# Optimization experiments

Hardware: AMD Instinct MI355X
Metric: run time of the kernel (lower is better)

The kernel has to match this reference:

```python
import jax, jax.numpy as jnp
import numpy as np

H = 16
D_MODEL = 1024
D_K = D_MODEL // H


def setup_inputs() -> dict:
    key = jax.random.key(0)
    ks = jax.random.split(key, 8)
    B, S = 4, 2048
    query = jax.random.normal(ks[0], (B, S, D_MODEL), dtype=jnp.float32)
    key_t = jax.random.normal(ks[1], (B, S, D_MODEL), dtype=jnp.float32)
    value = jax.random.normal(ks[2], (B, S, D_MODEL), dtype=jnp.float32)
    mask = jax.random.randint(ks[3], (B, S, S), 0, 2, dtype=jnp.int32)
    sc = 1.0 / np.sqrt(D_MODEL)
    Wq = jax.random.normal(ks[4], (D_MODEL, D_MODEL), dtype=jnp.float32) * sc
    Wk = jax.random.normal(ks[5], (D_MODEL, D_MODEL), dtype=jnp.float32) * sc
    Wv = jax.random.normal(ks[6], (D_MODEL, D_MODEL), dtype=jnp.float32) * sc
    Wo = jax.random.normal(ks[7], (D_MODEL, D_MODEL), dtype=jnp.float32) * sc
    return {"query": query, "key": key_t, "value": value, "mask": mask,
            "Wq": Wq, "Wk": Wk, "Wv": Wv, "Wo": Wo}


def reference(query, key, value, mask, Wq, Wk, Wv, Wo):
    B, S, _ = query.shape
    # nn.Linear(bias=False): y = x @ W^T; then split heads -> [B,H,S,d_k]
    def proj(x, W):
        return (x @ W.T).reshape(B, S, H, D_K).transpose(0, 2, 1, 3)

    q = proj(query, Wq)
    k = proj(key, Wk)
    v = proj(value, Wv)

    m = (mask[:, None, :, :] != 0)  # [B,1,S,S] broadcast over heads
    scores = jnp.einsum('bhqd,bhkd->bhqk', q, k) / jnp.sqrt(jnp.float32(D_K))
    scores = jnp.where(m, scores, jnp.float32(-1e9))
    p_attn = jax.nn.softmax(scores, axis=-1)
    p_attn = jnp.where(m, p_attn, 0.0)
    # dropout is identity in eval mode
    x = jnp.einsum('bhqk,bhkd->bhqd', p_attn, v)
    x = x.transpose(0, 2, 1, 3).reshape(B, S, D_MODEL)
    return x @ Wo.T
```

## Files before the change

kernel.cpp:

```cpp
#include <hip/hip_runtime.h>


typedef __attribute__((ext_vector_type(8))) short frag8;
typedef __attribute__((ext_vector_type(4))) float f32x4;
typedef unsigned long long ull;

#define MFMA16(a,b,c) __builtin_amdgcn_mfma_f32_16x16x32_bf16((a),(b),(c),0,0,0)

__device__ __forceinline__ short f2bf(float f) {
  union { float f; unsigned u; } x; x.f = f;
  unsigned r = (x.u + 0x7fffu + ((x.u >> 16) & 1u)) >> 16;
  return (short)r;
}

__device__ __forceinline__ unsigned pkbf(float lo, float hi) {
  union { float f; unsigned u; } a, b;
  a.f = lo; b.f = hi;
  return __builtin_amdgcn_perm(b.u + 0x8000u, a.u + 0x8000u, 0x07060302u);
}

__device__ __forceinline__ void gl16(const void* g, void* l) {
  __builtin_amdgcn_global_load_lds(
      (const __attribute__((address_space(1))) unsigned*)g,
      (__attribute__((address_space(3))) unsigned*)l, 16, 0, 0);
}

__global__ __launch_bounds__(256) void cast_qkv(
    const float* __restrict__ q, const float* __restrict__ k,
    const float* __restrict__ v, short* __restrict__ qo,
    short* __restrict__ ko, short* __restrict__ vo) {
  int z = blockIdx.x >> 13;
  int i = (blockIdx.x & 8191) * 256 + threadIdx.x;
  const float* s = z == 0 ? q : z == 1 ? k : v;
  short* d = z == 0 ? qo : z == 1 ? ko : vo;
  float4 f = ((const float4*)s)[i];
  short4 o;
  o.x = f2bf(f.x); o.y = f2bf(f.y); o.z = f2bf(f.z); o.w = f2bf(f.w);
  ((short4*)d)[i] = o;
}

__global__ __launch_bounds__(256) void cast_w(
    const float* __restrict__ wq, const float* __restrict__ wk,
    const float* __restrict__ wv, const float* __restrict__ wo,
    short* __restrict__ oq, short* __restrict__ ok,
    short* __restrict__ ov, short* __restrict__ oo) {
  int z = blockIdx.x >> 10;
  int i = (blockIdx.x & 1023) * 256 + threadIdx.x;
  const float* s = z == 0 ? wq : z == 1 ? wk : z == 2 ? wv : wo;
  short* d = z == 0 ? oq : z == 1 ? ok : z == 2 ? ov : oo;
  float sc = (z == 0) ? 0.18033688011f : 1.0f;
  float4 f = ((const float4*)s)[i];
  short4 o;
  o.x = f2bf(f.x * sc); o.y = f2bf(f.y * sc);
  o.z = f2bf(f.z * sc); o.w = f2bf(f.w * sc);
  ((short4*)d)[i] = o;
}

__global__ __launch_bounds__(256) void pack_mask(
    const int* __restrict__ mask, ull* __restrict__ bits) {
  int wv = threadIdx.x >> 6, l = threadIdx.x & 63;
  size_t row = (size_t)blockIdx.x * 4 + wv;
  const int* src = mask + row * 2048;
  for (int c = 0; c < 2048; c += 64) {
    ull bl = __ballot(src[c + l] != 0);
    if (l == 0) bits[row * 32 + (c >> 6)] = bl;
  }
}

template <int MODE>
__device__ __forceinline__ void gemm_body(const short* __restrict__ A,
                                          const short* __restrict__ W,
                                          void* __restrict__ outp, int bid) {
  __shared__ short As[2][128 * 32];
  __shared__ short Bs[2][128 * 32];
  const int t = threadIdx.x;
  const int l = t & 63, wv = t >> 6;
  const int lg = l >> 4, lr = l & 15;
  const int wm = (wv >> 1) * 64, wn = (wv & 1) * 64;
  const int m0 = (bid >> 3) * 128;
  const int n0 = (bid & 7) * 128;

  auto stage = [&](int buf, int kt) {
    const int k0 = kt * 32;
#pragma unroll
    for (int c = 0; c < 2; ++c) {
      int idx = c * 256 + t;
      int row = idx >> 2, ch = (idx & 3) * 8;
      gl16(A + (size_t)(m0 + row) * 1024 + k0 + ch, &As[buf][idx * 8]);
      gl16(W + (size_t)(n0 + row) * 1024 + k0 + ch, &Bs[buf][idx * 8]);
    }
  };

  f32x4 acc[4][4] = {};
  stage(0, 0);
  asm volatile("s_waitcnt vmcnt(0)" ::: "memory");
  __syncthreads();
  int buf = 0;
  for (int kt = 0; kt < 32; ++kt) {
    if (kt + 1 < 32) stage(buf ^ 1, kt + 1);
    frag8 af[4], bf[4];
#pragma unroll
    for (int i = 0; i < 4; ++i) {
      af[i] = *(const frag8*)&As[buf][(wm + i * 16 + lr) * 32 + 8 * lg];
      bf[i] = *(const frag8*)&Bs[buf][(wn + i * 16 + lr) * 32 + 8 * lg];
    }
    __builtin_amdgcn_s_setprio(1);
#pragma unroll
    for (int mi = 0; mi < 4; ++mi)
#pragma unroll
      for (int ni = 0; ni < 4; ++ni)
        acc[mi][ni] = MFMA16(af[mi], bf[ni], acc[mi][ni]);
    __builtin_amdgcn_s_setprio(0);
    asm volatile("s_waitcnt vmcnt(0)" ::: "memory");
    __syncthreads();
    buf ^= 1;
  }

#pragma unroll
  for (int mi = 0; mi < 4; ++mi)
#pragma unroll
    for (int ni = 0; ni < 4; ++ni)
#pragma unroll
      for (int r = 0; r < 4; ++r) {
        int m = m0 + wm + mi * 16 + 4 * lg + r;
        int n = n0 + wn + ni * 16 + lr;
        if (MODE == 0) {
          int b = m >> 11, s = m & 2047, h = n >> 6, dk = n & 63;
          ((short*)outp)[(((size_t)b * 16 + h) * 2048 + s) * 64 + dk] =
              f2bf(acc[mi][ni][r]);
        } else {
          ((float*)outp)[(size_t)m * 1024 + n] = acc[mi][ni][r];
        }
      }
}

__global__ __launch_bounds__(256) void gemm_qkv(
    const short* __restrict__ A0, const short* __restrict__ A1,
    const short* __restrict__ A2, const short* __restrict__ W0,
    const short* __restrict__ W1, const short* __restrict__ W2,
    short* __restrict__ O0, short* __restrict__ O1, short* __restrict__ O2) {
  int wg = (blockIdx.x & 7) * 192 + (blockIdx.x >> 3);
  int z = wg >> 9, bid = wg & 511;
  const short* A = z == 0 ? A0 : z == 1 ? A1 : A2;
  const short* W = z == 0 ? W0 : z == 1 ? W1 : W2;
  short* O = z == 0 ? O0 : z == 1 ? O1 : O2;
  gemm_body<0>(A, W, O, bid);
}

__global__ __launch_bounds__(256) void gemm_o(
    const short* __restrict__ A, const short* __restrict__ W,
    float* __restrict__ O) {
  int bid = (blockIdx.x & 7) * 64 + (blockIdx.x >> 3);
  gemm_body<1>(A, W, O, bid);
}

__global__ __launch_bounds__(256) void transpose_v(
    const short* __restrict__ Vp, short* __restrict__ Vt) {
  __shared__ short lds[64 * 72];
  int bh = blockIdx.y, s0 = blockIdx.x * 64;
  int t = threadIdx.x;
  int rr = t >> 3, c0 = (t & 7) * 8;
#pragma unroll
  for (int half = 0; half < 2; ++half) {
    int r = half * 32 + rr;
    frag8 v = *(const frag8*)(Vp + ((size_t)bh * 2048 + s0 + r) * 64 + c0);
#pragma unroll
    for (int j = 0; j < 8; ++j) lds[r * 72 + c0 + j] = v[j];
  }
  __syncthreads();
#pragma unroll
  for (int half = 0; half < 2; ++half) {
    int d = half * 32 + rr;
    frag8 o;
#pragma unroll
    for (int j = 0; j < 8; ++j) o[j] = lds[(c0 + j) * 72 + d];
    *(frag8*)(Vt + ((size_t)bh * 64 + d) * 2048 + s0 + c0) = o;
  }
}

__global__ __launch_bounds__(256, 4) void attn_fwd(
    const short* __restrict__ Qp, const short* __restrict__ Kp,
    const short* __restrict__ Vt, const ull* __restrict__ mb64,
    short* __restrict__ X) {
  __shared__ short Ks[2][64 * 64];
  __shared__ short Vs[64 * 64];
  __shared__ short Ps[4][32 * 64];

  const int wg = (blockIdx.x & 7) * 128 + (blockIdx.x >> 3);
  const int qt = wg & 15, bh = wg >> 4;
  const int b = bh >> 4, h = bh & 15;
  const int t = threadIdx.x;
  const int l = t & 63, wv = t >> 6;
  const int lg = l >> 4, lr = l & 15;
  const int q0 = qt * 128 + wv * 32;
  const int qrow_base = b << 11;

  frag8 qf[2][2];
  const short* Qb = Qp + ((size_t)bh * 2048 + q0) * 64;
#pragma unroll
  for (int qb = 0; qb < 2; ++qb)
#pragma unroll
    for (int kc = 0; kc < 2; ++kc)
      qf[qb][kc] = *(const frag8*)(Qb + (qb * 16 + lr) * 64 + kc * 32 + 8 * lg);

  f32x4 acc[4][2] = {};
  float mrun[2] = {0.f, 0.f}, lrun[2] = {0.f, 0.f};

  const size_t kbase = (size_t)bh * 2048 * 64;
  const size_t vbase = (size_t)bh * 64 * 2048;
  short* Pw = &Ps[wv][0];
  const int sx = lr & 7;

  auto stageK = [&](int buf, int kt) {
#pragma unroll
    for (int p = 0; p < 2; ++p) {
      int idx = p * 256 + t;
      int row = idx >> 3, c = idx & 7;
      int cs = (c ^ (row & 7)) * 8;
      gl16(Kp + kbase + (size_t)(kt * 64 + row) * 64 + cs, &Ks[buf][idx * 8]);
    }
  };
  auto stageV = [&](int kt) {
#pragma unroll
    for (int p = 0; p < 2; ++p) {
      int idx = p * 256 + t;
      int row = idx >> 3, c = idx & 7;
      int cs = (c ^ (row & 7)) * 8;
      gl16(Vt + vbase + (size_t)row * 2048 + kt * 64 + cs, &Vs[idx * 8]);
    }
  };

  stageK(0, 0);
  asm volatile("s_waitcnt vmcnt(0)" ::: "memory");
  __syncthreads();
  int buf = 0;

  for (int kt = 0; kt < 32; ++kt) {
    stageV(kt);
    stageK(buf ^ 1, (kt + 1) & 31);
    ull mw[2];
    mw[0] = mb64[(size_t)(qrow_base + q0 + lr) * 32 + kt];
    mw[1] = mb64[(size_t)(qrow_base + q0 + 16 + lr) * 32 + kt];

    f32x4 s[4][2] = {};
    __builtin_amdgcn_s_setprio(1);
#pragma unroll
    for (int nb = 0; nb < 4; ++nb) {
      const int ro = (nb * 16 + lr) * 64;
      frag8 k0 = *(const frag8*)&Ks[buf][ro + ((0 + lg) ^ sx) * 8];
      frag8 k1 = *(const frag8*)&Ks[buf][ro + ((4 + lg) ^ sx) * 8];
#pragma unroll
      for (int qb = 0; qb < 2; ++qb) {
        s[nb][qb] = MFMA16(k0, qf[qb][0], s[nb][qb]);
        s[nb][qb] = MFMA16(k1, qf[qb][1], s[nb][qb]);
      }
    }
    __builtin_amdgcn_s_setprio(0);

#pragma unroll
    for (int qb = 0; qb < 2; ++qb) {
      float pv[4][4];
      float tm = -1e30f;
#pragma unroll
      for (int nb = 0; nb < 4; ++nb) {
        unsigned nib = (unsigned)(mw[qb] >> (nb * 16 + 4 * lg)) & 0xFu;
#pragma unroll
        for (int r = 0; r < 4; ++r)
          pv[nb][r] = ((nib >> r) & 1u) ? s[nb][qb][r] : -1e30f;
        tm = fmaxf(fmaxf(fmaxf(pv[nb][0], pv[nb][1]),
                         fmaxf(pv[nb][2], pv[nb][3])), tm);
      }
      tm = fmaxf(tm, __shfl_xor(tm, 16));
      tm = fmaxf(tm, __shfl_xor(tm, 32));
      float mn = mrun[qb];
      float fac = 1.f;
      bool resc = !__all(tm - mn <= 11.0f);
      if (resc) {
        mn = fmaxf(mn, tm);
        fac = __builtin_amdgcn_exp2f(mrun[qb] - mn);
        mrun[qb] = mn;
      }
      float ts = 0.f;
      const int q64 = (qb * 16 + lr) * 64;
#pragma unroll
      for (int nb = 0; nb < 4; ++nb) {
        float e0 = __builtin_amdgcn_exp2f(pv[nb][0] - mn);
        float e1 = __builtin_amdgcn_exp2f(pv[nb][1] - mn);
        float e2 = __builtin_amdgcn_exp2f(pv[nb][2] - mn);
        float e3 = __builtin_amdgcn_exp2f(pv[nb][3] - mn);
        ts += (e0 + e1) + (e2 + e3);
        uint2 w;
        w.x = pkbf(e0, e1);
        w.y = pkbf(e2, e3);
        int sw = ((2 * nb + (lg >> 1)) ^ sx) * 8 + 4 * (lg & 1);
        *(uint2*)&Pw[q64 + sw] = w;
      }
      ts += __shfl_xor(ts, 16);
      ts += __shfl_xor(ts, 32);
      if (resc) {
        lrun[qb] = lrun[qb] * fac + ts;
#pragma unroll
        for (int db = 0; db < 4; ++db)
#pragma unroll
          for (int j = 0; j < 4; ++j) acc[db][qb][j] *= fac;
      } else {
        lrun[qb] += ts;
      }
    }

    asm volatile("s_waitcnt vmcnt(2)" ::: "memory");
    __syncthreads();

    frag8 pf[2][2];
#pragma unroll
    for (int qb = 0; qb < 2; ++qb)
#pragma unroll
      for (int kc = 0; kc < 2; ++kc)
        pf[qb][kc] = *(const frag8*)&Pw[(qb * 16 + lr) * 64 +
                                        ((kc * 4 + lg) ^ sx) * 8];
    __builtin_amdgcn_s_setprio(1);
#pragma unroll
    for (int db = 0; db < 4; ++db) {
      const int ro = (db * 16 + lr) * 64;
      frag8 v0 = *(const frag8*)&Vs[ro + ((0 + lg) ^ sx) * 8];
      frag8 v1 = *(const frag8*)&Vs[ro + ((4 + lg) ^ sx) * 8];
#pragma unroll
      for (int qb = 0; qb < 2; ++qb) {
        acc[db][qb] = MFMA16(v0, pf[qb][0], acc[db][qb]);
        acc[db][qb] = MFMA16(v1, pf[qb][1], acc[db][qb]);
      }
    }
    __builtin_amdgcn_s_setprio(0);

    asm volatile("s_waitcnt vmcnt(0)" ::: "memory");
    __syncthreads();
    buf ^= 1;
  }

#pragma unroll
  for (int qb = 0; qb < 2; ++qb) {
    float inv = 1.0f / fmaxf(lrun[qb], 1e-30f);
    int q = q0 + qb * 16 + lr;
    size_t base = (size_t)(qrow_base + q) * 1024 + h * 64 + 4 * lg;
#pragma unroll
    for (int db = 0; db < 4; ++db) {
      uint2 o;
      o.x = pkbf(acc[db][qb][0] * inv, acc[db][qb][1] * inv);
      o.y = pkbf(acc[db][qb][2] * inv, acc[db][qb][3] * inv);
      *(uint2*)&X[base + db * 16] = o;
    }
  }
}

extern "C" void kernel_launch(void* const* d_in, const int* in_sizes, int n_in,
                              void* d_out, int out_size, void* d_ws,
                              size_t ws_size, hipStream_t stream) {
  const float* q  = (const float*)d_in[0];
  const float* k  = (const float*)d_in[1];
  const float* v  = (const float*)d_in[2];
  const int*  msk = (const int*)d_in[3];
  const float* Wq = (const float*)d_in[4];
  const float* Wk = (const float*)d_in[5];
  const float* Wv = (const float*)d_in[6];
  const float* Wo = (const float*)d_in[7];

  const size_t SZ_T = 16777216;
  const size_t SZ_W = 2097152;
  char* ws = (char*)d_ws;
  short* qb  = (short*)(ws + 0 * SZ_T);
  short* kb  = (short*)(ws + 1 * SZ_T);
  short* vb  = (short*)(ws + 2 * SZ_T);
  short* Qp  = (short*)(ws + 3 * SZ_T);
  short* Kp  = (short*)(ws + 4 * SZ_T);
  short* Vp  = (short*)(ws + 5 * SZ_T);
  short* Vt  = (short*)(ws + 6 * SZ_T);
  short* X   = (short*)(ws + 7 * SZ_T);
  short* wqb = (short*)(ws + 8 * SZ_T);
  short* wkb = (short*)(ws + 8 * SZ_T + 1 * SZ_W);
  short* wvb = (short*)(ws + 8 * SZ_T + 2 * SZ_W);
  short* wob = (short*)(ws + 8 * SZ_T + 3 * SZ_W);
  void*  mb  = (void*)(ws + 8 * SZ_T + 4 * SZ_W);
  if (ws_size < 8 * SZ_T + 5 * SZ_W) return;

  cast_qkv<<<24576, 256, 0, stream>>>(q, k, v, qb, kb, vb);
  cast_w<<<4096, 256, 0, stream>>>(Wq, Wk, Wv, Wo, wqb, wkb, wvb, wob);
  pack_mask<<<2048, 256, 0, stream>>>(msk, (ull*)mb);

  gemm_qkv<<<1536, 256, 0, stream>>>(qb, kb, vb, wqb, wkb, wvb, Qp, Kp, Vp);
  transpose_v<<<dim3(32, 64), 256, 0, stream>>>(Vp, Vt);
  attn_fwd<<<1024, 256, 0, stream>>>(Qp, Kp, Vt, (const ull*)mb, X);
  gemm_o<<<512, 256, 0, stream>>>(X, wob, (float*)d_out);
}
```

Measured before the change: 291.9 us.

## Pre-expand mask to bf16 lane masks and apply via AND in attention

Replaces the bit-packed mask with a precomputed per-lane 16-bit expanded mask, laid out to match the MFMA output fragment. The attention kernel then applies the mask with a bitwise AND on the packed bf16 probabilities, and computes the row sum from those masked values. This removes the per-element select and bit extraction from the softmax inner loop. The cost is a mask buffer of about 32 MB, in a workspace region reused from dead buffers, which the attention kernel must read instead of 2 MB of bits. The row max now also covers masked scores, which changes the stabilisation offset but not the normalised result.

```diff
diff --git a/kernel.cpp b/kernel.cpp
--- a/kernel.cpp
+++ b/kernel.cpp
@@ -56,14 +56,26 @@
   ((short4*)d)[i] = o;
 }
 
-__global__ __launch_bounds__(256) void pack_mask(
-    const int* __restrict__ mask, ull* __restrict__ bits) {
-  int wv = threadIdx.x >> 6, l = threadIdx.x & 63;
-  size_t row = (size_t)blockIdx.x * 4 + wv;
-  const int* src = mask + row * 2048;
-  for (int c = 0; c < 2048; c += 64) {
-    ull bl = __ballot(src[c + l] != 0);
-    if (l == 0) bits[row * 32 + (c >> 6)] = bl;
+__global__ __launch_bounds__(256) void mask_expand(
+    const int* __restrict__ mask, uint2* __restrict__ mexp) {
+  int bgrp = blockIdx.x >> 2;
+  int kq = blockIdx.x & 3;
+  int b = bgrp >> 6, g = bgrp & 63;
+  int t = threadIdx.x;
+  int l = t & 63, nb = t >> 6;
+  int lg = l >> 4, lr = l & 15;
+#pragma unroll
+  for (int qb = 0; qb < 2; ++qb) {
+    const int* row = mask + ((size_t)b * 2048 + g * 32 + qb * 16 + lr) * 2048;
+#pragma unroll
+    for (int i = 0; i < 8; ++i) {
+      int kt = kq * 8 + i;
+      int4 m = *(const int4*)(row + kt * 64 + nb * 16 + lg * 4);
+      uint2 w;
+      w.x = (m.x ? 0xFFFFu : 0u) | (m.y ? 0xFFFF0000u : 0u);
+      w.y = (m.z ? 0xFFFFu : 0u) | (m.w ? 0xFFFF0000u : 0u);
+      mexp[((size_t)bgrp * 32 + kt) * 512 + (qb * 4 + nb) * 64 + l] = w;
+    }
   }
 }
 
@@ -180,7 +192,7 @@
 
 __global__ __launch_bounds__(256, 4) void attn_fwd(
     const short* __restrict__ Qp, const short* __restrict__ Kp,
-    const short* __restrict__ Vt, const ull* __restrict__ mb64,
+    const short* __restrict__ Vt, const uint2* __restrict__ mexp,
     short* __restrict__ X) {
   __shared__ short Ks[2][64 * 64];
   __shared__ short Vs[64 * 64];
@@ -210,6 +222,7 @@
   const size_t vbase = (size_t)bh * 64 * 2048;
   short* Pw = &Ps[wv][0];
   const int sx = lr & 7;
+  const uint2* mrow = mexp + ((size_t)(b * 64 + qt * 4 + wv) * 32) * 512 + l;
 
   auto stageK = [&](int buf, int kt) {
 #pragma unroll
@@ -236,11 +249,16 @@
   int buf = 0;
 
   for (int kt = 0; kt < 32; ++kt) {
+    uint2 mk[2][4];
+    const uint2* mt = mrow + kt * 512;
+#pragma unroll
+    for (int qb = 0; qb < 2; ++qb)
+#pragma unroll
+      for (int nb = 0; nb < 4; ++nb) mk[qb][nb] = mt[(qb * 4 + nb) * 64];
+    asm volatile("" ::: "memory");
     stageV(kt);
+    asm volatile("" ::: "memory");
     stageK(buf ^ 1, (kt + 1) & 31);
-    ull mw[2];
-    mw[0] = mb64[(size_t)(qrow_base + q0 + lr) * 32 + kt];
-    mw[1] = mb64[(size_t)(qrow_base + q0 + 16 + lr) * 32 + kt];
 
     f32x4 s[4][2] = {};
     __builtin_amdgcn_s_setprio(1);
@@ -259,17 +277,11 @@
 
 #pragma unroll
     for (int qb = 0; qb < 2; ++qb) {
-      float pv[4][4];
       float tm = -1e30f;
 #pragma unroll
-      for (int nb = 0; nb < 4; ++nb) {
-        unsigned nib = (unsigned)(mw[qb] >> (nb * 16 + 4 * lg)) & 0xFu;
-#pragma unroll
-        for (int r = 0; r < 4; ++r)
-          pv[nb][r] = ((nib >> r) & 1u) ? s[nb][qb][r] : -1e30f;
-        tm = fmaxf(fmaxf(fmaxf(pv[nb][0], pv[nb][1]),
-                         fmaxf(pv[nb][2], pv[nb][3])), tm);
-      }
+      for (int nb = 0; nb < 4; ++nb)
+        tm = fmaxf(tm, fmaxf(fmaxf(s[nb][qb][0], s[nb][qb][1]),
+                             fmaxf(s[nb][qb][2], s[nb][qb][3])));
       tm = fmaxf(tm, __shfl_xor(tm, 16));
       tm = fmaxf(tm, __shfl_xor(tm, 32));
       float mn = mrun[qb];
@@ -284,14 +296,15 @@
       const int q64 = (qb * 16 + lr) * 64;
 #pragma unroll
       for (int nb = 0; nb < 4; ++nb) {
-        float e0 = __builtin_amdgcn_exp2f(pv[nb][0] - mn);
-        float e1 = __builtin_amdgcn_exp2f(pv[nb][1] - mn);
-        float e2 = __builtin_amdgcn_exp2f(pv[nb][2] - mn);
-        float e3 = __builtin_amdgcn_exp2f(pv[nb][3] - mn);
-        ts += (e0 + e1) + (e2 + e3);
-        uint2 w;
-        w.x = pkbf(e0, e1);
-        w.y = pkbf(e2, e3);
+        float e0 = __builtin_amdgcn_exp2f(s[nb][qb][0] - mn);
+        float e1 = __builtin_amdgcn_exp2f(s[nb][qb][1] - mn);
+        float e2 = __builtin_amdgcn_exp2f(s[nb][qb][2] - mn);
+        float e3 = __builtin_amdgcn_exp2f(s[nb][qb][3] - mn);
+        unsigned w0 = pkbf(e0, e1) & mk[qb][nb].x;
+        unsigned w1 = pkbf(e2, e3) & mk[qb][nb].y;
+        ts += __uint_as_float(w0 << 16) + __uint_as_float(w0 & 0xFFFF0000u) +
+              __uint_as_float(w1 << 16) + __uint_as_float(w1 & 0xFFFF0000u);
+        uint2 w; w.x = w0; w.y = w1;
         int sw = ((2 * nb + (lg >> 1)) ^ sx) * 8 + 4 * (lg & 1);
         *(uint2*)&Pw[q64 + sw] = w;
       }
@@ -379,15 +392,14 @@
   short* wkb = (short*)(ws + 8 * SZ_T + 1 * SZ_W);
   short* wvb = (short*)(ws + 8 * SZ_T + 2 * SZ_W);
   short* wob = (short*)(ws + 8 * SZ_T + 3 * SZ_W);
-  void*  mb  = (void*)(ws + 8 * SZ_T + 4 * SZ_W);
-  if (ws_size < 8 * SZ_T + 5 * SZ_W) return;
+  void*  mexp = (void*)(ws + 0 * SZ_T);
+  if (ws_size < 8 * SZ_T + 4 * SZ_W) return;
 
   cast_qkv<<<24576, 256, 0, stream>>>(q, k, v, qb, kb, vb);
   cast_w<<<4096, 256, 0, stream>>>(Wq, Wk, Wv, Wo, wqb, wkb, wvb, wob);
-  pack_mask<<<2048, 256, 0, stream>>>(msk, (ull*)mb);
-
   gemm_qkv<<<1536, 256, 0, stream>>>(qb, kb, vb, wqb, wkb, wvb, Qp, Kp, Vp);
+  mask_expand<<<1024, 256, 0, stream>>>(msk, (uint2*)mexp);
   transpose_v<<<dim3(32, 64), 256, 0, stream>>>(Vp, Vt);
-  attn_fwd<<<1024, 256, 0, stream>>>(Qp, Kp, Vt, (const ull*)mb, X);
+  attn_fwd<<<1024, 256, 0, stream>>>(Qp, Kp, Vt, (const uint2*)mexp, X);
   gemm_o<<<512, 256, 0, stream>>>(X, wob, (float*)d_out);
 }
```

New measurement: 289.5 us. Within noise of the previous version (-0.8%).
